# Performance work log

Measured on AMD Instinct MI355X. Metric: run time of the kernel, lower is better.

## Reference

```python
import jax, jax.numpy as jnp
import numpy as np

B, S, D = 4, 2048, 1024
O = 1024
E = 8
K = 2

def setup_inputs() -> dict:
    key = jax.random.key(0)
    k1, k2, k3, k4, k5 = jax.random.split(key, 5)
    scale = 1.0 / np.sqrt(D)
    x = jax.random.normal(k1, (B, S, D), dtype=jnp.float32)
    # expert linear layers stacked: weight [E, D, O], bias [E, O]
    We = jax.random.uniform(k2, (E, D, O), dtype=jnp.float32, minval=-scale, maxval=scale)
    be = jax.random.uniform(k3, (E, O), dtype=jnp.float32, minval=-scale, maxval=scale)
    # gate linear: weight [D, E], bias [E]
    Wg = jax.random.uniform(k4, (D, E), dtype=jnp.float32, minval=-scale, maxval=scale)
    bg = jax.random.uniform(k5, (E,), dtype=jnp.float32, minval=-scale, maxval=scale)
    return {"x": x, "We": We, "be": be, "Wg": Wg, "bg": bg}

def reference(x, We, be, Wg, bg):
    b, s, d = x.shape
    x_flat = x.reshape(-1, d)                                   # [N, D]
    gates = jax.nn.softmax(x_flat @ Wg + bg, axis=-1)           # [N, E]
    topk_gates, topk_idx = jax.lax.top_k(gates, K)              # [N, K]
    topk_gates = topk_gates / jnp.sum(topk_gates, axis=1, keepdims=True)
    # dense all-expert compute (faithful to original naive MoE)
    expert_out = jnp.einsum('nd,edo->neo', x_flat, We) + be     # [N, E, O]
    # gather top-k expert outputs per token
    selected = jnp.take_along_axis(expert_out, topk_idx[:, :, None], axis=1)  # [N, K, O]
    out = jnp.sum(selected * topk_gates[:, :, None], axis=1)    # [N, O]
    return out.reshape(b, s, -1)
```

## Files before the change

kernel.cpp:

```cpp
#include <hip/hip_runtime.h>

#define N_TOK 8192
#define DDIM 1024
#define ODIM 1024
#define NEXP 8

typedef __attribute__((ext_vector_type(8))) short bf16x8;
typedef __attribute__((ext_vector_type(4))) float f32x4;

__device__ __forceinline__ unsigned int f2bf(float f) {
    unsigned int u = __float_as_uint(f);
    return (u + 0x7fffu + ((u >> 16) & 1u)) >> 16;
}
__device__ __forceinline__ float bflo(unsigned int u) { return __uint_as_float(u << 16); }
__device__ __forceinline__ float bfhi(unsigned int u) { return __uint_as_float(u & 0xffff0000u); }

__device__ __forceinline__ void async_copy16(const unsigned short* g, unsigned short* l) {
    __builtin_amdgcn_global_load_lds(
        (const __attribute__((address_space(1))) unsigned int*)g,
        (__attribute__((address_space(3))) unsigned int*)l, 16, 0, 0);
}

__global__ __launch_bounds__(256) void prep_kernel(const float* __restrict__ x,
                                                   const float* __restrict__ Wg,
                                                   const float* __restrict__ bg,
                                                   const float* __restrict__ We,
                                                   int* __restrict__ ea, int* __restrict__ eb,
                                                   float* __restrict__ ga, float* __restrict__ gb,
                                                   unsigned short* __restrict__ xbf,
                                                   unsigned short* __restrict__ WeT,
                                                   int* __restrict__ counts) {
    __shared__ float tile[64][65];
    if (blockIdx.x < 2048) {
        if (blockIdx.x == 0) counts[threadIdx.x] = 0;
        const int wave = threadIdx.x >> 6, lane = threadIdx.x & 63;
        const int t = blockIdx.x * 4 + wave;
        const float* xr = x + (size_t)t * DDIM;

        float4 v[4];
#pragma unroll
        for (int c = 0; c < 4; ++c) v[c] = *(const float4*)&xr[c * 256 + lane * 4];

        unsigned short* xo = xbf + (size_t)t * DDIM;
#pragma unroll
        for (int c = 0; c < 4; ++c) {
            uint2 w;
            w.x = f2bf(v[c].x) | (f2bf(v[c].y) << 16);
            w.y = f2bf(v[c].z) | (f2bf(v[c].w) << 16);
            *(uint2*)&xo[c * 256 + lane * 4] = w;
        }

        float acc[8] = {0, 0, 0, 0, 0, 0, 0, 0};
#pragma unroll
        for (int c = 0; c < 4; ++c) {
            const int dbase = c * 256 + lane * 4;
#pragma unroll
            for (int j = 0; j < 4; ++j) {
                float xv = ((const float*)&v[c])[j];
                const float4* w = (const float4*)(Wg + (size_t)(dbase + j) * 8);
                float4 w0 = w[0], w1 = w[1];
                acc[0] += xv * w0.x; acc[1] += xv * w0.y; acc[2] += xv * w0.z; acc[3] += xv * w0.w;
                acc[4] += xv * w1.x; acc[5] += xv * w1.y; acc[6] += xv * w1.z; acc[7] += xv * w1.w;
            }
        }
#pragma unroll
        for (int off = 32; off > 0; off >>= 1) {
#pragma unroll
            for (int j = 0; j < 8; ++j) acc[j] += __shfl_xor(acc[j], off, 64);
        }
        if (lane == 0) {
            float s[8];
#pragma unroll
            for (int e = 0; e < 8; ++e) s[e] = acc[e] + bg[e];
            int a = 0;
#pragma unroll
            for (int e = 1; e < 8; ++e) if (s[e] > s[a]) a = e;
            int b = (a == 0) ? 1 : 0;
#pragma unroll
            for (int e = 0; e < 8; ++e) if (e != a && e != b && s[e] > s[b]) b = e;
            float g0 = 1.0f / (1.0f + __expf(s[b] - s[a]));
            ea[t] = a; eb[t] = b; ga[t] = g0; gb[t] = 1.0f - g0;
        }
    } else {
        const int lin = blockIdx.x - 2048;
        const int e = lin >> 8, rem = lin & 255;
        const int d0 = (rem >> 4) * 64, o0 = (rem & 15) * 64;
        const int tid = threadIdx.x;
#pragma unroll
        for (int p = 0; p < 4; ++p) {
            int idx = p * 256 + tid;
            int row = idx >> 4, c = idx & 15;
            float4 v = *(const float4*)&We[(((size_t)e * 1024 + d0 + row) << 10) + o0 + (c << 2)];
            tile[row][c * 4 + 0] = v.x; tile[row][c * 4 + 1] = v.y;
            tile[row][c * 4 + 2] = v.z; tile[row][c * 4 + 3] = v.w;
        }
        __syncthreads();
#pragma unroll
        for (int p = 0; p < 2; ++p) {
            int idx = p * 256 + tid;
            int orow = idx >> 3, c8 = idx & 7;
            unsigned int u[8];
#pragma unroll
            for (int j = 0; j < 8; ++j) u[j] = f2bf(tile[c8 * 8 + j][orow]);
            uint4 q;
            q.x = u[0] | (u[1] << 16); q.y = u[2] | (u[3] << 16);
            q.z = u[4] | (u[5] << 16); q.w = u[6] | (u[7] << 16);
            *(uint4*)&WeT[(((size_t)e * 1024 + o0 + orow) << 10) + d0 + (c8 << 3)] = q;
        }
    }
}

__global__ __launch_bounds__(64) void scatter_kernel(const int* __restrict__ ea,
                                                     const int* __restrict__ eb,
                                                     int* __restrict__ counts,
                                                     int* __restrict__ btok,
                                                     int* __restrict__ slotA,
                                                     int* __restrict__ slotB) {
    const int t = blockIdx.x * 64 + threadIdx.x;
    const int lane = threadIdx.x & 63;
#pragma unroll
    for (int pass = 0; pass < 2; ++pass) {
        const int e = (pass == 0) ? ea[t] : eb[t];
        int* slot = (pass == 0) ? slotA : slotB;
#pragma unroll
        for (int ex = 0; ex < NEXP; ++ex) {
            unsigned long long mask = __ballot(e == ex);
            if (mask) {
                int leader = __ffsll((long long)mask) - 1;
                int base = 0;
                if (lane == leader) base = atomicAdd(&counts[ex * 32], __popcll(mask));
                base = __shfl(base, leader, 64);
                if (e == ex) {
                    int pos = base + __popcll(mask & ((1ull << lane) - 1ull));
                    btok[ex * N_TOK + pos] = t;
                    slot[t] = ex * N_TOK + pos;
                }
            }
        }
    }
}

__global__ __launch_bounds__(256, 2) void moe_gemm(const unsigned short* __restrict__ xbf,
                                                   const unsigned short* __restrict__ WeT,
                                                   const float* __restrict__ be,
                                                   const int* __restrict__ counts,
                                                   const int* __restrict__ btok,
                                                   unsigned short* __restrict__ ybuf) {
    const int id = blockIdx.x;
    const int e = id & 7;
    const int n0 = ((id >> 3) & 7) * 128;
    const int r0 = (id >> 6) * 128;
    const int cnt = counts[e * 32];
    if (r0 >= cnt) return;

    __shared__ unsigned short smem[32768];
    __shared__ int s_tok[128];

    const int tid = threadIdx.x;
    if (tid < 128) {
        int r = r0 + tid;
        int rc = (r < cnt) ? r : (cnt - 1);
        s_tok[tid] = btok[e * N_TOK + rc];
    }
    const int w = tid >> 6, lane = tid & 63;
    __syncthreads();

    const int rsub = lane >> 3;
    const int colo = ((lane & 7) ^ rsub) * 8;
    unsigned int a_off[4], b_off[4];
#pragma unroll
    for (int p = 0; p < 4; ++p) {
        int row = p * 32 + w * 8 + rsub;
        a_off[p] = ((unsigned)s_tok[row] << 10) + colo;
        b_off[p] = ((unsigned)(e * 1024 + n0 + row) << 10) + colo;
    }
    const int ldsrow = w * 8;

    const int wm = (w >> 1) * 64, wn = (w & 1) * 64;
    const int quad = lane >> 4, rA = lane & 15;
    const int sw = rA & 7;
    const int cs0 = (quad ^ sw) * 8;
    const int cs1 = ((4 + quad) ^ sw) * 8;

    f32x4 acc[4][4];
#pragma unroll
    for (int mi = 0; mi < 4; ++mi)
#pragma unroll
        for (int ni = 0; ni < 4; ++ni) acc[mi][ni] = (f32x4){0.f, 0.f, 0.f, 0.f};

#pragma unroll
    for (int p = 0; p < 4; ++p) {
        async_copy16(xbf + a_off[p], &smem[(p * 32 + ldsrow) * 64]);
        async_copy16(WeT + b_off[p], &smem[16384 + (p * 32 + ldsrow) * 64]);
    }
#pragma unroll
    for (int p = 0; p < 4; ++p) {
        async_copy16(xbf + a_off[p] + 64, &smem[8192 + (p * 32 + ldsrow) * 64]);
        async_copy16(WeT + b_off[p] + 64, &smem[24576 + (p * 32 + ldsrow) * 64]);
    }
    asm volatile("s_waitcnt vmcnt(8)" ::: "memory");
    __builtin_amdgcn_s_barrier();
    __builtin_amdgcn_sched_barrier(0);

    for (int t = 0; t < 16; ++t) {
        const int cur = t & 1;
        unsigned short* sAc = smem + cur * 8192;
        unsigned short* sBc = smem + 16384 + cur * 8192;

        bf16x8 a0[4], b0[4];
#pragma unroll
        for (int mi = 0; mi < 4; ++mi) a0[mi] = *(bf16x8*)&sAc[(wm + mi * 16 + rA) * 64 + cs0];
#pragma unroll
        for (int ni = 0; ni < 4; ++ni) b0[ni] = *(bf16x8*)&sBc[(wn + ni * 16 + rA) * 64 + cs0];
        asm volatile("s_waitcnt lgkmcnt(0)" ::: "memory");
        __builtin_amdgcn_sched_barrier(0);

        __builtin_amdgcn_s_setprio(1);
#pragma unroll
        for (int mi = 0; mi < 4; ++mi)
#pragma unroll
            for (int ni = 0; ni < 4; ++ni)
                acc[mi][ni] = __builtin_amdgcn_mfma_f32_16x16x32_bf16(b0[ni], a0[mi], acc[mi][ni], 0, 0, 0);
        __builtin_amdgcn_s_setprio(0);

        bf16x8 a1[4], b1[4];
#pragma unroll
        for (int mi = 0; mi < 4; ++mi) a1[mi] = *(bf16x8*)&sAc[(wm + mi * 16 + rA) * 64 + cs1];
#pragma unroll
        for (int ni = 0; ni < 4; ++ni) b1[ni] = *(bf16x8*)&sBc[(wn + ni * 16 + rA) * 64 + cs1];
        asm volatile("s_waitcnt lgkmcnt(0)" ::: "memory");
        __builtin_amdgcn_sched_barrier(0);
        __builtin_amdgcn_s_barrier();
        __builtin_amdgcn_sched_barrier(0);

        if (t < 14) {
            const int ko = (t + 2) * 64;
#pragma unroll
            for (int p = 0; p < 4; ++p) {
                async_copy16(xbf + a_off[p] + ko, &sAc[(p * 32 + ldsrow) * 64]);
                async_copy16(WeT + b_off[p] + ko, &sBc[(p * 32 + ldsrow) * 64]);
            }
        }

        __builtin_amdgcn_s_setprio(1);
#pragma unroll
        for (int mi = 0; mi < 4; ++mi)
#pragma unroll
            for (int ni = 0; ni < 4; ++ni)
                acc[mi][ni] = __builtin_amdgcn_mfma_f32_16x16x32_bf16(b1[ni], a1[mi], acc[mi][ni], 0, 0, 0);
        __builtin_amdgcn_s_setprio(0);

        if (t < 14) {
            asm volatile("s_waitcnt vmcnt(8)" ::: "memory");
            __builtin_amdgcn_s_barrier();
            __builtin_amdgcn_sched_barrier(0);
        } else if (t == 14) {
            asm volatile("s_waitcnt vmcnt(0)" ::: "memory");
            __builtin_amdgcn_s_barrier();
            __builtin_amdgcn_sched_barrier(0);
        }
    }

#pragma unroll
    for (int mi = 0; mi < 4; ++mi) {
        const int lrow = wm + mi * 16 + rA;
        if (r0 + lrow < cnt) {
            unsigned short* yrow =
                ybuf + (((size_t)(e * N_TOK + r0 + lrow)) << 10) + n0 + wn + quad * 4;
#pragma unroll
            for (int ni = 0; ni < 4; ++ni) {
                float4 bv = *(const float4*)&be[(e << 10) + n0 + wn + ni * 16 + quad * 4];
                uint2 pk;
                pk.x = f2bf(acc[mi][ni][0] + bv.x) | (f2bf(acc[mi][ni][1] + bv.y) << 16);
                pk.y = f2bf(acc[mi][ni][2] + bv.z) | (f2bf(acc[mi][ni][3] + bv.w) << 16);
                *(uint2*)&yrow[ni * 16] = pk;
            }
        }
    }
}

__global__ __launch_bounds__(256) void combine_kernel(const unsigned short* __restrict__ ybuf,
                                                      const int* __restrict__ slotA,
                                                      const int* __restrict__ slotB,
                                                      const float* __restrict__ ga,
                                                      const float* __restrict__ gb,
                                                      float* __restrict__ out) {
    const int wave = threadIdx.x >> 6, lane = threadIdx.x & 63;
    const int t = blockIdx.x * 4 + wave;
    const unsigned short* ra = ybuf + ((size_t)slotA[t] << 10);
    const unsigned short* rb = ybuf + ((size_t)slotB[t] << 10);
    const float a = ga[t], b = gb[t];
    float* orow = out + ((size_t)t << 10);
#pragma unroll
    for (int i = 0; i < 2; ++i) {
        int c = i * 512 + lane * 8;
        uint4 ua = *(const uint4*)&ra[c];
        uint4 ub = *(const uint4*)&rb[c];
        float4 o0, o1;
        o0.x = a * bflo(ua.x) + b * bflo(ub.x);
        o0.y = a * bfhi(ua.x) + b * bfhi(ub.x);
        o0.z = a * bflo(ua.y) + b * bflo(ub.y);
        o0.w = a * bfhi(ua.y) + b * bfhi(ub.y);
        o1.x = a * bflo(ua.z) + b * bflo(ub.z);
        o1.y = a * bfhi(ua.z) + b * bfhi(ub.z);
        o1.z = a * bflo(ua.w) + b * bflo(ub.w);
        o1.w = a * bfhi(ua.w) + b * bfhi(ub.w);
        *(float4*)&orow[c] = o0;
        *(float4*)&orow[c + 4] = o1;
    }
}

extern "C" void kernel_launch(void* const* d_in, const int* in_sizes, int n_in,
                              void* d_out, int out_size, void* d_ws, size_t ws_size,
                              hipStream_t stream) {
    const float* x  = (const float*)d_in[0];
    const float* We = (const float*)d_in[1];
    const float* be = (const float*)d_in[2];
    const float* Wg = (const float*)d_in[3];
    const float* bg = (const float*)d_in[4];
    float* out = (float*)d_out;

    char* ws = (char*)d_ws;
    size_t off = 0;
    int* counts = (int*)(ws + off); off += 8 * 32 * 4;
    int* btok   = (int*)(ws + off); off += NEXP * N_TOK * 4;
    int* slotA  = (int*)(ws + off); off += N_TOK * 4;
    int* slotB  = (int*)(ws + off); off += N_TOK * 4;
    int* ea = (int*)(ws + off); off += N_TOK * 4;
    int* eb = (int*)(ws + off); off += N_TOK * 4;
    float* ga = (float*)(ws + off); off += N_TOK * 4;
    float* gb = (float*)(ws + off); off += N_TOK * 4;
    unsigned short* WeT  = (unsigned short*)(ws + off); off += (size_t)NEXP * DDIM * ODIM * 2;
    unsigned short* xbf  = (unsigned short*)(ws + off); off += (size_t)N_TOK * DDIM * 2;
    unsigned short* ybuf = (unsigned short*)(ws + off); off += (size_t)NEXP * N_TOK * ODIM * 2;

    prep_kernel<<<dim3(4096), 256, 0, stream>>>(x, Wg, bg, We, ea, eb, ga, gb, xbf, WeT, counts);
    scatter_kernel<<<dim3(N_TOK / 64), 64, 0, stream>>>(ea, eb, counts, btok, slotA, slotB);
    moe_gemm<<<dim3(64 * 8 * 8), 256, 0, stream>>>(xbf, WeT, be, counts, btok, ybuf);
    combine_kernel<<<dim3(N_TOK / 4), 256, 0, stream>>>(ybuf, slotA, slotB, ga, gb, out);
}
```

Measured before the change: 214.3 us.

## Software-pipeline LDS fragment loads across k-steps and split prep kernel

```diff
diff --git a/kernel.cpp b/kernel.cpp
--- a/kernel.cpp
+++ b/kernel.cpp
@@ -21,92 +21,91 @@
         (__attribute__((address_space(3))) unsigned int*)l, 16, 0, 0);
 }
 
-__global__ __launch_bounds__(256) void prep_kernel(const float* __restrict__ x,
+__global__ __launch_bounds__(256) void gate_kernel(const float* __restrict__ x,
                                                    const float* __restrict__ Wg,
                                                    const float* __restrict__ bg,
-                                                   const float* __restrict__ We,
                                                    int* __restrict__ ea, int* __restrict__ eb,
                                                    float* __restrict__ ga, float* __restrict__ gb,
                                                    unsigned short* __restrict__ xbf,
-                                                   unsigned short* __restrict__ WeT,
                                                    int* __restrict__ counts) {
+    if (blockIdx.x == 0) counts[threadIdx.x] = 0;
+    const int wave = threadIdx.x >> 6, lane = threadIdx.x & 63;
+    const int t = blockIdx.x * 4 + wave;
+    const float* xr = x + (size_t)t * DDIM;
+
+    float4 v[4];
+#pragma unroll
+    for (int c = 0; c < 4; ++c) v[c] = *(const float4*)&xr[c * 256 + lane * 4];
+
+    unsigned short* xo = xbf + (size_t)t * DDIM;
+#pragma unroll
+    for (int c = 0; c < 4; ++c) {
+        uint2 w;
+        w.x = f2bf(v[c].x) | (f2bf(v[c].y) << 16);
+        w.y = f2bf(v[c].z) | (f2bf(v[c].w) << 16);
+        *(uint2*)&xo[c * 256 + lane * 4] = w;
+    }
+
+    float acc[8] = {0, 0, 0, 0, 0, 0, 0, 0};
+#pragma unroll
+    for (int c = 0; c < 4; ++c) {
+        const int dbase = c * 256 + lane * 4;
+#pragma unroll
+        for (int j = 0; j < 4; ++j) {
+            float xv = ((const float*)&v[c])[j];
+            const float4* w = (const float4*)(Wg + (size_t)(dbase + j) * 8);
+            float4 w0 = w[0], w1 = w[1];
+            acc[0] += xv * w0.x; acc[1] += xv * w0.y; acc[2] += xv * w0.z; acc[3] += xv * w0.w;
+            acc[4] += xv * w1.x; acc[5] += xv * w1.y; acc[6] += xv * w1.z; acc[7] += xv * w1.w;
+        }
+    }
+#pragma unroll
+    for (int off = 32; off > 0; off >>= 1) {
+#pragma unroll
+        for (int j = 0; j < 8; ++j) acc[j] += __shfl_xor(acc[j], off, 64);
+    }
+    if (lane == 0) {
+        float s[8];
+#pragma unroll
+        for (int e = 0; e < 8; ++e) s[e] = acc[e] + bg[e];
+        int a = 0;
+#pragma unroll
+        for (int e = 1; e < 8; ++e) if (s[e] > s[a]) a = e;
+        int b = (a == 0) ? 1 : 0;
+#pragma unroll
+        for (int e = 0; e < 8; ++e) if (e != a && e != b && s[e] > s[b]) b = e;
+        float g0 = 1.0f / (1.0f + __expf(s[b] - s[a]));
+        ea[t] = a; eb[t] = b; ga[t] = g0; gb[t] = 1.0f - g0;
+    }
+}
+
+__global__ __launch_bounds__(256) void transpose_kernel(const float* __restrict__ We,
+                                                        unsigned short* __restrict__ WeT) {
     __shared__ float tile[64][65];
-    if (blockIdx.x < 2048) {
-        if (blockIdx.x == 0) counts[threadIdx.x] = 0;
-        const int wave = threadIdx.x >> 6, lane = threadIdx.x & 63;
-        const int t = blockIdx.x * 4 + wave;
-        const float* xr = x + (size_t)t * DDIM;
-
-        float4 v[4];
-#pragma unroll
-        for (int c = 0; c < 4; ++c) v[c] = *(const float4*)&xr[c * 256 + lane * 4];
-
-        unsigned short* xo = xbf + (size_t)t * DDIM;
-#pragma unroll
-        for (int c = 0; c < 4; ++c) {
-            uint2 w;
-            w.x = f2bf(v[c].x) | (f2bf(v[c].y) << 16);
-            w.y = f2bf(v[c].z) | (f2bf(v[c].w) << 16);
-            *(uint2*)&xo[c * 256 + lane * 4] = w;
-        }
-
-        float acc[8] = {0, 0, 0, 0, 0, 0, 0, 0};
-#pragma unroll
-        for (int c = 0; c < 4; ++c) {
-            const int dbase = c * 256 + lane * 4;
-#pragma unroll
-            for (int j = 0; j < 4; ++j) {
-                float xv = ((const float*)&v[c])[j];
-                const float4* w = (const float4*)(Wg + (size_t)(dbase + j) * 8);
-                float4 w0 = w[0], w1 = w[1];
-                acc[0] += xv * w0.x; acc[1] += xv * w0.y; acc[2] += xv * w0.z; acc[3] += xv * w0.w;
-                acc[4] += xv * w1.x; acc[5] += xv * w1.y; acc[6] += xv * w1.z; acc[7] += xv * w1.w;
-            }
-        }
-#pragma unroll
-        for (int off = 32; off > 0; off >>= 1) {
-#pragma unroll
-            for (int j = 0; j < 8; ++j) acc[j] += __shfl_xor(acc[j], off, 64);
-        }
-        if (lane == 0) {
-            float s[8];
-#pragma unroll
-            for (int e = 0; e < 8; ++e) s[e] = acc[e] + bg[e];
-            int a = 0;
-#pragma unroll
-            for (int e = 1; e < 8; ++e) if (s[e] > s[a]) a = e;
-            int b = (a == 0) ? 1 : 0;
-#pragma unroll
-            for (int e = 0; e < 8; ++e) if (e != a && e != b && s[e] > s[b]) b = e;
-            float g0 = 1.0f / (1.0f + __expf(s[b] - s[a]));
-            ea[t] = a; eb[t] = b; ga[t] = g0; gb[t] = 1.0f - g0;
-        }
-    } else {
-        const int lin = blockIdx.x - 2048;
-        const int e = lin >> 8, rem = lin & 255;
-        const int d0 = (rem >> 4) * 64, o0 = (rem & 15) * 64;
-        const int tid = threadIdx.x;
-#pragma unroll
-        for (int p = 0; p < 4; ++p) {
-            int idx = p * 256 + tid;
-            int row = idx >> 4, c = idx & 15;
-            float4 v = *(const float4*)&We[(((size_t)e * 1024 + d0 + row) << 10) + o0 + (c << 2)];
-            tile[row][c * 4 + 0] = v.x; tile[row][c * 4 + 1] = v.y;
-            tile[row][c * 4 + 2] = v.z; tile[row][c * 4 + 3] = v.w;
-        }
-        __syncthreads();
-#pragma unroll
-        for (int p = 0; p < 2; ++p) {
-            int idx = p * 256 + tid;
-            int orow = idx >> 3, c8 = idx & 7;
-            unsigned int u[8];
-#pragma unroll
-            for (int j = 0; j < 8; ++j) u[j] = f2bf(tile[c8 * 8 + j][orow]);
-            uint4 q;
-            q.x = u[0] | (u[1] << 16); q.y = u[2] | (u[3] << 16);
-            q.z = u[4] | (u[5] << 16); q.w = u[6] | (u[7] << 16);
-            *(uint4*)&WeT[(((size_t)e * 1024 + o0 + orow) << 10) + d0 + (c8 << 3)] = q;
-        }
+    const int lin = blockIdx.x;
+    const int e = lin >> 8, rem = lin & 255;
+    const int d0 = (rem >> 4) * 64, o0 = (rem & 15) * 64;
+    const int tid = threadIdx.x;
+#pragma unroll
+    for (int p = 0; p < 4; ++p) {
+        int idx = p * 256 + tid;
+        int row = idx >> 4, c = idx & 15;
+        float4 v = *(const float4*)&We[(((size_t)e * 1024 + d0 + row) << 10) + o0 + (c << 2)];
+        tile[row][c * 4 + 0] = v.x; tile[row][c * 4 + 1] = v.y;
+        tile[row][c * 4 + 2] = v.z; tile[row][c * 4 + 3] = v.w;
+    }
+    __syncthreads();
+#pragma unroll
+    for (int p = 0; p < 2; ++p) {
+        int idx = p * 256 + tid;
+        int orow = idx >> 3, c8 = idx & 7;
+        unsigned int u[8];
+#pragma unroll
+        for (int j = 0; j < 8; ++j) u[j] = f2bf(tile[c8 * 8 + j][orow]);
+        uint4 q;
+        q.x = u[0] | (u[1] << 16); q.y = u[2] | (u[3] << 16);
+        q.z = u[4] | (u[5] << 16); q.w = u[6] | (u[7] << 16);
+        *(uint4*)&WeT[(((size_t)e * 1024 + o0 + orow) << 10) + d0 + (c8 << 3)] = q;
     }
 }
 
@@ -202,19 +201,26 @@
     __builtin_amdgcn_s_barrier();
     __builtin_amdgcn_sched_barrier(0);
 
+    bf16x8 a0[4], b0[4];
+#pragma unroll
+    for (int i = 0; i < 4; ++i) {
+        a0[i] = *(bf16x8*)&smem[(wm + i * 16 + rA) * 64 + cs0];
+        b0[i] = *(bf16x8*)&smem[16384 + (wn + i * 16 + rA) * 64 + cs0];
+    }
+
     for (int t = 0; t < 16; ++t) {
         const int cur = t & 1;
         unsigned short* sAc = smem + cur * 8192;
         unsigned short* sBc = smem + 16384 + cur * 8192;
-
-        bf16x8 a0[4], b0[4];
-#pragma unroll
-        for (int mi = 0; mi < 4; ++mi) a0[mi] = *(bf16x8*)&sAc[(wm + mi * 16 + rA) * 64 + cs0];
-#pragma unroll
-        for (int ni = 0; ni < 4; ++ni) b0[ni] = *(bf16x8*)&sBc[(wn + ni * 16 + rA) * 64 + cs0];
-        asm volatile("s_waitcnt lgkmcnt(0)" ::: "memory");
-        __builtin_amdgcn_sched_barrier(0);
-
+        unsigned short* sAn = smem + (cur ^ 1) * 8192;
+        unsigned short* sBn = smem + 16384 + (cur ^ 1) * 8192;
+
+        bf16x8 a1[4], b1[4];
+#pragma unroll
+        for (int i = 0; i < 4; ++i) {
+            a1[i] = *(bf16x8*)&sAc[(wm + i * 16 + rA) * 64 + cs1];
+            b1[i] = *(bf16x8*)&sBc[(wn + i * 16 + rA) * 64 + cs1];
+        }
         __builtin_amdgcn_s_setprio(1);
 #pragma unroll
         for (int mi = 0; mi < 4; ++mi)
@@ -223,11 +229,6 @@
                 acc[mi][ni] = __builtin_amdgcn_mfma_f32_16x16x32_bf16(b0[ni], a0[mi], acc[mi][ni], 0, 0, 0);
         __builtin_amdgcn_s_setprio(0);
 
-        bf16x8 a1[4], b1[4];
-#pragma unroll
-        for (int mi = 0; mi < 4; ++mi) a1[mi] = *(bf16x8*)&sAc[(wm + mi * 16 + rA) * 64 + cs1];
-#pragma unroll
-        for (int ni = 0; ni < 4; ++ni) b1[ni] = *(bf16x8*)&sBc[(wn + ni * 16 + rA) * 64 + cs1];
         asm volatile("s_waitcnt lgkmcnt(0)" ::: "memory");
         __builtin_amdgcn_sched_barrier(0);
         __builtin_amdgcn_s_barrier();
@@ -241,6 +242,21 @@
                 async_copy16(WeT + b_off[p] + ko, &sBc[(p * 32 + ldsrow) * 64]);
             }
         }
+        if (t < 15) {
+            if (t < 14) {
+                asm volatile("s_waitcnt vmcnt(8)" ::: "memory");
+            } else {
+                asm volatile("s_waitcnt vmcnt(0)" ::: "memory");
+            }
+            __builtin_amdgcn_sched_barrier(0);
+            __builtin_amdgcn_s_barrier();
+            __builtin_amdgcn_sched_barrier(0);
+#pragma unroll
+            for (int i = 0; i < 4; ++i) {
+                a0[i] = *(bf16x8*)&sAn[(wm + i * 16 + rA) * 64 + cs0];
+                b0[i] = *(bf16x8*)&sBn[(wn + i * 16 + rA) * 64 + cs0];
+            }
+        }
 
         __builtin_amdgcn_s_setprio(1);
 #pragma unroll
@@ -249,18 +265,12 @@
             for (int ni = 0; ni < 4; ++ni)
                 acc[mi][ni] = __builtin_amdgcn_mfma_f32_16x16x32_bf16(b1[ni], a1[mi], acc[mi][ni], 0, 0, 0);
         __builtin_amdgcn_s_setprio(0);
-
-        if (t < 14) {
-            asm volatile("s_waitcnt vmcnt(8)" ::: "memory");
-            __builtin_amdgcn_s_barrier();
-            __builtin_amdgcn_sched_barrier(0);
-        } else if (t == 14) {
-            asm volatile("s_waitcnt vmcnt(0)" ::: "memory");
-            __builtin_amdgcn_s_barrier();
-            __builtin_amdgcn_sched_barrier(0);
-        }
-    }
-
+    }
+
+    float4 bv[4];
+#pragma unroll
+    for (int ni = 0; ni < 4; ++ni)
+        bv[ni] = *(const float4*)&be[(e << 10) + n0 + wn + ni * 16 + quad * 4];
 #pragma unroll
     for (int mi = 0; mi < 4; ++mi) {
         const int lrow = wm + mi * 16 + rA;
@@ -269,10 +279,9 @@
                 ybuf + (((size_t)(e * N_TOK + r0 + lrow)) << 10) + n0 + wn + quad * 4;
 #pragma unroll
             for (int ni = 0; ni < 4; ++ni) {
-                float4 bv = *(const float4*)&be[(e << 10) + n0 + wn + ni * 16 + quad * 4];
                 uint2 pk;
-                pk.x = f2bf(acc[mi][ni][0] + bv.x) | (f2bf(acc[mi][ni][1] + bv.y) << 16);
-                pk.y = f2bf(acc[mi][ni][2] + bv.z) | (f2bf(acc[mi][ni][3] + bv.w) << 16);
+                pk.x = f2bf(acc[mi][ni][0] + bv[ni].x) | (f2bf(acc[mi][ni][1] + bv[ni].y) << 16);
+                pk.y = f2bf(acc[mi][ni][2] + bv[ni].z) | (f2bf(acc[mi][ni][3] + bv[ni].w) << 16);
                 *(uint2*)&yrow[ni * 16] = pk;
             }
         }
@@ -334,7 +343,8 @@
     unsigned short* xbf  = (unsigned short*)(ws + off); off += (size_t)N_TOK * DDIM * 2;
     unsigned short* ybuf = (unsigned short*)(ws + off); off += (size_t)NEXP * N_TOK * ODIM * 2;
 
-    prep_kernel<<<dim3(4096), 256, 0, stream>>>(x, Wg, bg, We, ea, eb, ga, gb, xbf, WeT, counts);
+    gate_kernel<<<dim3(2048), 256, 0, stream>>>(x, Wg, bg, ea, eb, ga, gb, xbf, counts);
+    transpose_kernel<<<dim3(2048), 256, 0, stream>>>(We, WeT);
     scatter_kernel<<<dim3(N_TOK / 64), 64, 0, stream>>>(ea, eb, counts, btok, slotA, slotB);
     moe_gemm<<<dim3(64 * 8 * 8), 256, 0, stream>>>(xbf, WeT, be, counts, btok, ybuf);
     combine_kernel<<<dim3(N_TOK / 4), 256, 0, stream>>>(ybuf, slotA, slotB, ga, gb, out);
```

Result: no change. 217.8 us (+1.6%).
